# Kernel tuning notes

Measured on AMD Instinct MI355X. Metric: run time of the kernel, lower is better.

The kernel has to match this reference:

```python
import jax, jax.numpy as jnp
import numpy as np

NBINS = 128
LOGSCALE = False


def setup_inputs() -> dict:
    key = jax.random.key(0)
    X = jax.random.normal(key, (2048, 32768), dtype=jnp.float32)
    return {"X": X}


def reference(X) -> jnp.ndarray:
    # Flatten all non-leading dims (mirrors X.view(len(X), -1))
    X = X.reshape(X.shape[0], -1)
    ns = X.shape[1]
    nfreqs = 2 * (NBINS - 1) + 1          # window length (255)
    hop = nfreqs // 2
    starts = jnp.arange(0, ns - nfreqs + 1, hop)          # [nwin]
    idx = starts[:, None] + jnp.arange(nfreqs)[None, :]    # [nwin, nfreqs]
    W = X[:, idx]                          # [ntrials, nwin, nfreqs] gathered windows
    # One batched rfft + fused |.|^2 and mean over windows (Welch average)
    S = jnp.mean(jnp.abs(jnp.fft.rfft(W, axis=-1)) ** 2, axis=1)  # [ntrials, NBINS]
    if LOGSCALE:
        S = jnp.log10(S)
    return S
```

## Files before the change

kernel.cpp:

```cpp
#include <hip/hip_runtime.h>
#include <hip/hip_bf16.h>

#define NS     32768
#define NROWS  2048
#define HOP    127
#define NW     257
#define NB     128
#define WTILE  16
#define NT     17
#define TWOPI_255 0.02463994236f

typedef _Float16 f16;
typedef __attribute__((ext_vector_type(8))) _Float16 f16x8;
typedef __attribute__((ext_vector_type(4))) float f32x4;

__device__ inline f32x4 load4u(const float* p) {
    f32x4 v;
    __builtin_memcpy(&v, p, 16);
    return v;
}

__global__ __launch_bounds__(256, 4)
void psd_fold_kernel(const float* __restrict__ X, float* __restrict__ out) {
    const int row  = blockIdx.x;
    const int tid  = threadIdx.x;
    const int lane = tid & 63;
    const int cq   = tid >> 6;
    const int r16  = lane & 15;
    const int kg   = lane >> 4;
    const int is_sin = cq >> 1;

    __shared__ alignas(16) f16 atile[2][WTILE * 256];
    __shared__ float scol[256];

    const float* __restrict__ xrow = X + (size_t)row * NS;

    const int sw  = tid >> 4;
    const int sk0 = (tid & 15) * 8;

    f32x4 fva, fvb, rva, rvb;
    {
        const int b = sw * HOP;
        fva = load4u(xrow + b + sk0);
        fvb = load4u(xrow + b + sk0 + 4);
        rva = load4u(xrow + b + 248 - sk0);
        rvb = load4u(xrow + b + 252 - sk0);
    }

    f16x8 bfrag[4][4];
    #pragma unroll
    for (int nt = 0; nt < 4; ++nt) {
        const int comp = cq * 64 + nt * 16 + r16;
        const int f    = comp & 127;
        #pragma unroll
        for (int kk = 0; kk < 4; ++kk) {
            int m = (f * (kk * 32 + kg * 8)) % 255;
            f16x8 v;
            #pragma unroll
            for (int j = 0; j < 8; ++j) {
                const float ang = (float)m * TWOPI_255;
                const float s   = is_sin ? __sinf(ang) : __cosf(ang);
                v[j] = (f16)s;
                m += f; if (m >= 255) m -= 255;
            }
            bfrag[nt][kk] = v;
        }
    }

    const f16x8 z8 = {(f16)0,(f16)0,(f16)0,(f16)0,(f16)0,(f16)0,(f16)0,(f16)0};
    auto fold_write = [&](int buf, bool valid, f32x4 fa, f32x4 fb, f32x4 ra, f32x4 rb) {
        float yp[8], ym[8];
        #pragma unroll
        for (int j = 0; j < 8; ++j) {
            const float fj = (j < 4) ? fa[j] : fb[j - 4];
            const int   pi = 7 - j;
            const float rj = (pi < 4) ? ra[pi] : rb[pi - 4];
            yp[j] = fj + rj;
            ym[j] = fj - rj;
        }
        if (sk0 == 0) { yp[0] = fa[0]; ym[0] = 0.0f; }
        f16x8 h0, h1;
        #pragma unroll
        for (int j = 0; j < 8; ++j) { h0[j] = (f16)yp[j]; h1[j] = (f16)ym[j]; }
        if (!valid) { h0 = z8; h1 = z8; }
        char* wp = (char*)&atile[buf][0];
        const uint sb  = (uint)(sw * 512 + sk0 * 2);
        const uint swz = (uint)((sw & 7) << 4);
        *(f16x8*)(wp + (sb ^ swz))         = h0;
        *(f16x8*)(wp + ((sb + 256) ^ swz)) = h1;
    };

    fold_write(0, true, fva, fvb, rva, rvb);
    __syncthreads();

    float ssum[4] = {0.f, 0.f, 0.f, 0.f};
    const uint rswz  = (uint)((r16 & 7) << 4);
    const uint rbase = (uint)(r16 * 512 + is_sin * 256 + kg * 16);

    for (int mt = 0; mt < NT; ++mt) {
        const int  cur       = mt & 1;
        const bool have_next = (mt + 1 < NT);
        bool nvalid = false;
        if (have_next) {
            const int w = (mt + 1) * WTILE + sw;
            nvalid = (w < NW);
            int b = w * HOP; if (b > NS - 256) b = NS - 256;
            fva = load4u(xrow + b + sk0);
            fvb = load4u(xrow + b + sk0 + 4);
            rva = load4u(xrow + b + 248 - sk0);
            rvb = load4u(xrow + b + 252 - sk0);
        }

        const char* ap = (const char*)&atile[cur][0];
        f32x4 acc0 = {0,0,0,0}, acc1 = {0,0,0,0}, acc2 = {0,0,0,0}, acc3 = {0,0,0,0};
        #pragma unroll
        for (int kk = 0; kk < 4; ++kk) {
            const f16x8 af = *(const f16x8*)(ap + ((rbase + (uint)(kk * 64)) ^ rswz));
            acc0 = __builtin_amdgcn_mfma_f32_16x16x32_f16(af, bfrag[0][kk], acc0, 0, 0, 0);
            acc1 = __builtin_amdgcn_mfma_f32_16x16x32_f16(af, bfrag[1][kk], acc1, 0, 0, 0);
            acc2 = __builtin_amdgcn_mfma_f32_16x16x32_f16(af, bfrag[2][kk], acc2, 0, 0, 0);
            acc3 = __builtin_amdgcn_mfma_f32_16x16x32_f16(af, bfrag[3][kk], acc3, 0, 0, 0);
        }
        #pragma unroll
        for (int r = 0; r < 4; ++r) {
            ssum[0] += acc0[r] * acc0[r];
            ssum[1] += acc1[r] * acc1[r];
            ssum[2] += acc2[r] * acc2[r];
            ssum[3] += acc3[r] * acc3[r];
        }

        if (have_next) fold_write(cur ^ 1, nvalid, fva, fvb, rva, rvb);
        __syncthreads();
    }

    #pragma unroll
    for (int nt = 0; nt < 4; ++nt) {
        float v = ssum[nt];
        v += __shfl_xor(v, 16, 64);
        v += __shfl_xor(v, 32, 64);
        if (kg == 0) scol[cq * 64 + nt * 16 + r16] = v;
    }
    __syncthreads();
    if (tid < NB) {
        out[(size_t)row * NB + tid] = (scol[tid] + scol[tid + NB]) * (1.0f / 257.0f);
    }
}

extern "C" void kernel_launch(void* const* d_in, const int* in_sizes, int n_in,
                              void* d_out, int out_size, void* d_ws, size_t ws_size,
                              hipStream_t stream) {
    const float* X = (const float*)d_in[0];
    float* out = (float*)d_out;
    (void)in_sizes; (void)n_in; (void)d_ws; (void)ws_size; (void)out_size;
    psd_fold_kernel<<<dim3(NROWS), dim3(256), 0, stream>>>(X, out);
}
```

Baseline: 66.85 us.

## Deepen global prefetch to two tiles ahead and precompute LDS offsets

Global loads for the window tile two steps ahead are now issued right after the fold-write of the next tile, so loads have a full iteration of MFMA work to hide behind instead of being issued just before compute. LDS read/write swizzled offsets are hoisted out of the loop, fp16 conversion uses packed cvt_pkrtz, and the MFMA block is wrapped in s_setprio. Address clamping via min on byte offsets replaces per-iteration branch logic. Round-toward-zero conversion slightly changes rounding versus the prior default conversion.

After: 216.5 us. 3.24x slower.

```diff
diff --git a/kernel.cpp b/kernel.cpp
--- a/kernel.cpp
+++ b/kernel.cpp
@@ -11,17 +11,18 @@
 #define TWOPI_255 0.02463994236f
 
 typedef _Float16 f16;
+typedef __attribute__((ext_vector_type(2))) _Float16 f16x2;
 typedef __attribute__((ext_vector_type(8))) _Float16 f16x8;
 typedef __attribute__((ext_vector_type(4))) float f32x4;
 
-__device__ inline f32x4 load4u(const float* p) {
+__device__ inline f32x4 load4u(const char* p) {
     f32x4 v;
     __builtin_memcpy(&v, p, 16);
     return v;
 }
 
 __global__ __launch_bounds__(256, 4)
-void psd_fold_kernel(const float* __restrict__ X, float* __restrict__ out) {
+void psd_kernel(const float* __restrict__ X, float* __restrict__ out) {
     const int row  = blockIdx.x;
     const int tid  = threadIdx.x;
     const int lane = tid & 63;
@@ -33,19 +34,19 @@
     __shared__ alignas(16) f16 atile[2][WTILE * 256];
     __shared__ float scol[256];
 
-    const float* __restrict__ xrow = X + (size_t)row * NS;
+    const char* __restrict__ xrow = (const char*)(X + (size_t)row * NS);
 
     const int sw  = tid >> 4;
     const int sk0 = (tid & 15) * 8;
 
-    f32x4 fva, fvb, rva, rvb;
-    {
-        const int b = sw * HOP;
-        fva = load4u(xrow + b + sk0);
-        fvb = load4u(xrow + b + sk0 + 4);
-        rva = load4u(xrow + b + 248 - sk0);
-        rvb = load4u(xrow + b + 252 - sk0);
-    }
+    const uint voff_fwd = (uint)((sw * HOP + sk0) * 4);
+    const uint voff_rev = (uint)((sw * HOP + 248 - sk0) * 4);
+    const uint vclamp   = (uint)((NS - 4) * 4);
+
+    f32x4 fva = load4u(xrow + voff_fwd);
+    f32x4 fvb = load4u(xrow + voff_fwd + 16);
+    f32x4 rva = load4u(xrow + voff_rev);
+    f32x4 rvb = load4u(xrow + voff_rev + 16);
 
     f16x8 bfrag[4][4];
     #pragma unroll
@@ -59,68 +60,79 @@
             #pragma unroll
             for (int j = 0; j < 8; ++j) {
                 const float ang = (float)m * TWOPI_255;
-                const float s   = is_sin ? __sinf(ang) : __cosf(ang);
-                v[j] = (f16)s;
+                v[j] = (f16)(is_sin ? __sinf(ang) : __cosf(ang));
                 m += f; if (m >= 255) m -= 255;
             }
             bfrag[nt][kk] = v;
         }
     }
 
-    const f16x8 z8 = {(f16)0,(f16)0,(f16)0,(f16)0,(f16)0,(f16)0,(f16)0,(f16)0};
-    auto fold_write = [&](int buf, bool valid, f32x4 fa, f32x4 fb, f32x4 ra, f32x4 rb) {
+    const uint swz  = (uint)((sw & 7) << 4);
+    const uint wr0  = (uint)(sw * 512 + sk0 * 2) ^ swz;
+    const uint wr1  = (uint)(sw * 512 + sk0 * 2 + 256) ^ swz;
+    const uint rswz = (uint)((r16 & 7) << 4);
+    uint rd[4];
+    #pragma unroll
+    for (int kk = 0; kk < 4; ++kk)
+        rd[kk] = (uint)(r16 * 512 + is_sin * 256 + kg * 16 + kk * 64) ^ rswz;
+
+    char* const lds = (char*)&atile[0][0];
+
+    auto fold_write = [&](uint bufoff, bool valid) {
         float yp[8], ym[8];
         #pragma unroll
         for (int j = 0; j < 8; ++j) {
-            const float fj = (j < 4) ? fa[j] : fb[j - 4];
+            const float fj = (j < 4) ? fva[j] : fvb[j - 4];
             const int   pi = 7 - j;
-            const float rj = (pi < 4) ? ra[pi] : rb[pi - 4];
+            const float rj = (pi < 4) ? rva[pi] : rvb[pi - 4];
             yp[j] = fj + rj;
             ym[j] = fj - rj;
         }
-        if (sk0 == 0) { yp[0] = fa[0]; ym[0] = 0.0f; }
+        if (sk0 == 0) { yp[0] = fva[0]; ym[0] = 0.0f; }
         f16x8 h0, h1;
         #pragma unroll
-        for (int j = 0; j < 8; ++j) { h0[j] = (f16)yp[j]; h1[j] = (f16)ym[j]; }
-        if (!valid) { h0 = z8; h1 = z8; }
-        char* wp = (char*)&atile[buf][0];
-        const uint sb  = (uint)(sw * 512 + sk0 * 2);
-        const uint swz = (uint)((sw & 7) << 4);
-        *(f16x8*)(wp + (sb ^ swz))         = h0;
-        *(f16x8*)(wp + ((sb + 256) ^ swz)) = h1;
+        for (int q = 0; q < 4; ++q) {
+            f16x2 pp = __builtin_bit_cast(f16x2, __builtin_amdgcn_cvt_pkrtz(yp[2*q], yp[2*q+1]));
+            f16x2 pm = __builtin_bit_cast(f16x2, __builtin_amdgcn_cvt_pkrtz(ym[2*q], ym[2*q+1]));
+            h0[2*q] = pp[0]; h0[2*q+1] = pp[1];
+            h1[2*q] = pm[0]; h1[2*q+1] = pm[1];
+        }
+        if (!valid) {
+            #pragma unroll
+            for (int q = 0; q < 8; ++q) { h0[q] = (f16)0.0f; h1[q] = (f16)0.0f; }
+        }
+        *(f16x8*)(lds + bufoff + wr0) = h0;
+        *(f16x8*)(lds + bufoff + wr1) = h1;
     };
 
-    fold_write(0, true, fva, fvb, rva, rvb);
+    fold_write(0u, true);
+    {
+        const uint ub = (uint)(1 * WTILE * HOP * 4);
+        fva = load4u(xrow + (voff_fwd + ub));
+        fvb = load4u(xrow + (voff_fwd + ub + 16));
+        rva = load4u(xrow + (voff_rev + ub));
+        rvb = load4u(xrow + (voff_rev + ub + 16));
+    }
     __syncthreads();
 
     float ssum[4] = {0.f, 0.f, 0.f, 0.f};
-    const uint rswz  = (uint)((r16 & 7) << 4);
-    const uint rbase = (uint)(r16 * 512 + is_sin * 256 + kg * 16);
 
+    #pragma unroll 2
     for (int mt = 0; mt < NT; ++mt) {
-        const int  cur       = mt & 1;
-        const bool have_next = (mt + 1 < NT);
-        bool nvalid = false;
-        if (have_next) {
-            const int w = (mt + 1) * WTILE + sw;
-            nvalid = (w < NW);
-            int b = w * HOP; if (b > NS - 256) b = NS - 256;
-            fva = load4u(xrow + b + sk0);
-            fvb = load4u(xrow + b + sk0 + 4);
-            rva = load4u(xrow + b + 248 - sk0);
-            rvb = load4u(xrow + b + 252 - sk0);
-        }
+        const uint bo_cur = (mt & 1) ? 8192u : 0u;
+        const uint bo_nxt = bo_cur ^ 8192u;
 
-        const char* ap = (const char*)&atile[cur][0];
         f32x4 acc0 = {0,0,0,0}, acc1 = {0,0,0,0}, acc2 = {0,0,0,0}, acc3 = {0,0,0,0};
+        __builtin_amdgcn_s_setprio(1);
         #pragma unroll
         for (int kk = 0; kk < 4; ++kk) {
-            const f16x8 af = *(const f16x8*)(ap + ((rbase + (uint)(kk * 64)) ^ rswz));
+            const f16x8 af = *(const f16x8*)(lds + bo_cur + rd[kk]);
             acc0 = __builtin_amdgcn_mfma_f32_16x16x32_f16(af, bfrag[0][kk], acc0, 0, 0, 0);
             acc1 = __builtin_amdgcn_mfma_f32_16x16x32_f16(af, bfrag[1][kk], acc1, 0, 0, 0);
             acc2 = __builtin_amdgcn_mfma_f32_16x16x32_f16(af, bfrag[2][kk], acc2, 0, 0, 0);
             acc3 = __builtin_amdgcn_mfma_f32_16x16x32_f16(af, bfrag[3][kk], acc3, 0, 0, 0);
         }
+        __builtin_amdgcn_s_setprio(0);
         #pragma unroll
         for (int r = 0; r < 4; ++r) {
             ssum[0] += acc0[r] * acc0[r];
@@ -129,7 +141,21 @@
             ssum[3] += acc3[r] * acc3[r];
         }
 
-        if (have_next) fold_write(cur ^ 1, nvalid, fva, fvb, rva, rvb);
+        if (mt < NT - 1) {
+            const bool valid = (mt != 15) || (sw == 0);
+            fold_write(bo_nxt, valid);
+        }
+        if (mt < NT - 2) {
+            const uint ub = (uint)((mt + 2) * WTILE * HOP * 4);
+            const uint f0 = min(voff_fwd + ub,      vclamp);
+            const uint f1 = min(voff_fwd + ub + 16, vclamp);
+            const uint r0 = min(voff_rev + ub,      vclamp);
+            const uint r1 = min(voff_rev + ub + 16, vclamp);
+            fva = load4u(xrow + f0);
+            fvb = load4u(xrow + f1);
+            rva = load4u(xrow + r0);
+            rvb = load4u(xrow + r1);
+        }
         __syncthreads();
     }
 
@@ -152,5 +178,5 @@
     const float* X = (const float*)d_in[0];
     float* out = (float*)d_out;
     (void)in_sizes; (void)n_in; (void)d_ws; (void)ws_size; (void)out_size;
-    psd_fold_kernel<<<dim3(NROWS), dim3(256), 0, stream>>>(X, out);
+    psd_kernel<<<dim3(NROWS), dim3(256), 0, stream>>>(X, out);
 }
```
